# Performance work log

Hardware: AMD Instinct MI355X
Metric: run time of the kernel (lower is better)

The kernel has to match this reference:

```python
import jax, jax.numpy as jnp
import numpy as np

C = 1024
RANK = 8


def _layernorm(x, g, b, eps=1e-5):
    mu = jnp.mean(x, axis=-1, keepdims=True)
    var = jnp.var(x, axis=-1, keepdims=True)
    return (x - mu) * jax.lax.rsqrt(var + eps) * g + b


def setup_inputs() -> dict:
    key = jax.random.key(0)
    ks = jax.random.split(key, 10)
    B, T = 4, 4096
    x = jax.random.normal(ks[0], (B, T, C), dtype=jnp.float32)
    # parameters (match torch inits)
    W0 = jnp.eye(C, dtype=jnp.float32) * 0.1
    A_init = jax.random.normal(ks[1], (C, RANK), dtype=jnp.float32) * 0.01
    B_init = jnp.zeros((RANK, C), dtype=jnp.float32)
    log_lr = jnp.full((C,), float(np.log(0.1)), dtype=jnp.float32)
    s = 1.0 / np.sqrt(C)
    Wq = jax.random.uniform(ks[2], (C, C), minval=-s, maxval=s, dtype=jnp.float32)
    Wk = jax.random.uniform(ks[3], (C, C), minval=-s, maxval=s, dtype=jnp.float32)
    Wv = jax.random.uniform(ks[4], (C, C), minval=-s, maxval=s, dtype=jnp.float32)
    Wo = jax.random.uniform(ks[5], (C, C), minval=-s, maxval=s, dtype=jnp.float32)
    Wg = jax.random.uniform(ks[6], (C, C), minval=-s, maxval=s, dtype=jnp.float32)
    ln_g = jnp.ones((C,), dtype=jnp.float32)
    ln_b = jnp.zeros((C,), dtype=jnp.float32)
    ls_g = jnp.full((C,), 1e-4, dtype=jnp.float32)  # LayerScale gamma
    return {"x": x, "W0": W0, "A_init": A_init, "B_init": B_init,
            "log_lr": log_lr, "Wq": Wq, "Wk": Wk, "Wv": Wv, "Wo": Wo,
            "Wg": Wg, "ln_g": ln_g, "ln_b": ln_b, "ls_g": ls_g}


def reference(x, W0, A_init, B_init, log_lr, Wq, Wk, Wv, Wo, Wg, ln_g, ln_b, ls_g):
    B, T, _ = x.shape
    h = _layernorm(x, ln_g, ln_b)
    # dual-form TTT (training path: q/k/v projections, full K @ W0)
    Q = jnp.einsum('btc,dc->btd', h, Wq)
    K = jnp.einsum('btc,dc->btd', h, Wk)
    V = jnp.einsum('btc,dc->btd', h, Wv)
    lr = jnp.minimum(jnp.exp(log_lr), 1.0)  # clamp(max=1.0)
    y0 = jnp.einsum('btc,cd->btd', K, W0) + jnp.einsum('btr,rd->btd', jnp.einsum('btc,cr->btr', K, A_init), B_init)
    error = y0 - V
    loss = jnp.mean(error ** 2)
    gradient = K * error                     # [B,T,C]
    grad_cumsum = jnp.cumsum(gradient, axis=1)
    grad_shift = jnp.concatenate([jnp.zeros((B, 1, gradient.shape[-1]), gradient.dtype), grad_cumsum[:, :-1, :]], axis=1)
    correction = Q * lr[None, None, :] * grad_shift
    pos = jnp.arange(1, T + 1, dtype=correction.dtype)
    pos_scale = (1.0 / (1.0 + 0.1 * jnp.log(pos)))[None, :, None]
    out = y0 - correction * pos_scale
    # gate, out projection, layer scale, residual
    gate = jax.nn.sigmoid(jnp.einsum('btc,dc->btd', x, Wg))
    out = out * gate
    out = jnp.einsum('btc,dc->btd', out, Wo) * ls_g
    return (x + out, loss)
```

## Files before the change

kernel.cpp:

```cpp
#include <hip/hip_runtime.h>
#include <stdint.h>
#include <math.h>

typedef unsigned short u16;
typedef __attribute__((ext_vector_type(8))) short short8;
typedef __attribute__((ext_vector_type(4))) float f32x4;

__device__ __forceinline__ float bf2f(u16 u){
  union { unsigned int i; float f; } v; v.i = ((unsigned int)u) << 16; return v.f;
}
__device__ __forceinline__ u16 f2bf(float f){
  union { float f; unsigned int i; } v; v.f = f;
  return (u16)((v.i + 0x7FFFu + ((v.i >> 16) & 1u)) >> 16);
}

__global__ void ln_prep(const float* __restrict__ x, const float* __restrict__ g,
                        const float* __restrict__ bta, u16* __restrict__ h,
                        u16* __restrict__ xb, float* __restrict__ loss){
  if (blockIdx.x == 0 && threadIdx.x == 0) loss[0] = 0.f;
  int row = blockIdx.x, tid = threadIdx.x;
  const float4* xr = (const float4*)(x + (size_t)row * 1024);
  float4 v = xr[tid];
  float s  = v.x + v.y + v.z + v.w;
  float s2 = v.x*v.x + v.y*v.y + v.z*v.z + v.w*v.w;
  #pragma unroll
  for (int o = 32; o > 0; o >>= 1){ s += __shfl_down(s, o); s2 += __shfl_down(s2, o); }
  __shared__ float red[8];
  if ((tid & 63) == 0){ red[tid >> 6] = s; red[4 + (tid >> 6)] = s2; }
  __syncthreads();
  float ts = red[0]+red[1]+red[2]+red[3];
  float t2 = red[4]+red[5]+red[6]+red[7];
  float mu   = ts * (1.0f/1024.0f);
  float var  = t2 * (1.0f/1024.0f) - mu*mu;
  float rstd = rsqrtf(var + 1e-5f);
  float4 gg = ((const float4*)g)[tid];
  float4 bb = ((const float4*)bta)[tid];
  ushort4 hv, xv;
  hv.x = f2bf((v.x-mu)*rstd*gg.x + bb.x);
  hv.y = f2bf((v.y-mu)*rstd*gg.y + bb.y);
  hv.z = f2bf((v.z-mu)*rstd*gg.z + bb.z);
  hv.w = f2bf((v.w-mu)*rstd*gg.w + bb.w);
  xv.x = f2bf(v.x); xv.y = f2bf(v.y); xv.z = f2bf(v.z); xv.w = f2bf(v.w);
  ((ushort4*)h )[(size_t)row*256 + tid] = hv;
  ((ushort4*)xb)[(size_t)row*256 + tid] = xv;
}

__global__ void conv5(const float* __restrict__ a, const float* __restrict__ b,
                      const float* __restrict__ c, const float* __restrict__ d,
                      const float* __restrict__ e,
                      u16* oa, u16* ob, u16* oc, u16* od, u16* oe){
  int sel = blockIdx.y;
  const float* s = sel==0?a : sel==1?b : sel==2?c : sel==3?d : e;
  u16* o = sel==0?oa : sel==1?ob : sel==2?oc : sel==3?od : oe;
  int i = blockIdx.x*256 + threadIdx.x;
  float4 v = ((const float4*)s)[i];
  ushort4 r; r.x=f2bf(v.x); r.y=f2bf(v.y); r.z=f2bf(v.z); r.w=f2bf(v.w);
  ((ushort4*)o)[i] = r;
}

__global__ void weff_k(const float* __restrict__ W0, const float* __restrict__ Ai,
                       const float* __restrict__ Bi, u16* __restrict__ Wet){
  __shared__ float tile[32][33];
  int d0 = blockIdx.x*32, e0 = blockIdx.y*32;
  int tid = threadIdx.x;
  int lr = tid >> 5, lc = tid & 31;
  #pragma unroll
  for (int s = 0; s < 4; ++s){
    int e = e0 + s*8 + lr, d = d0 + lc;
    float v = W0[(size_t)e*1024 + d];
    #pragma unroll
    for (int r = 0; r < 8; ++r) v += Ai[e*8 + r] * Bi[(size_t)r*1024 + d];
    tile[s*8 + lr][lc] = v;
  }
  __syncthreads();
  #pragma unroll
  for (int s = 0; s < 4; ++s){
    int d = d0 + s*8 + lr, e = e0 + lc;
    Wet[(size_t)d*1024 + e] = f2bf(tile[lc][s*8 + lr]);
  }
}

template<int EPI>
__device__ __forceinline__ void gemm_body(const u16* __restrict__ A, const u16* __restrict__ Bm,
    u16* __restrict__ Cb, float* __restrict__ Cf, const float* __restrict__ lsg,
    const float* __restrict__ xres, int mblk, int nblk){
  __shared__ u16 As[128*64];
  __shared__ u16 Bs[128*64];
  const int tid  = threadIdx.x;
  const int lane = tid & 63;
  const int w    = tid >> 6;
  const int m0 = mblk * 128, n0 = nblk * 128;
  const int lrow = lane >> 3, lcol8 = (lane & 7) * 8;
  const int wm = w & 1, wn = w >> 1;
  const int l15 = lane & 15, quad = lane >> 4;

  f32x4 acc[4][4] = {};

  #pragma unroll 1
  for (int kk = 0; kk < 1024; kk += 64){
    #pragma unroll
    for (int it = 0; it < 4; ++it){
      int r0 = w*8 + it*32;
      const u16* ga = A  + (size_t)(m0 + r0 + lrow)*1024 + kk + lcol8;
      __builtin_amdgcn_global_load_lds((const __attribute__((address_space(1))) unsigned int*)ga,
          (__attribute__((address_space(3))) unsigned int*)(As + r0*64), 16, 0, 0);
      const u16* gb = Bm + (size_t)(n0 + r0 + lrow)*1024 + kk + lcol8;
      __builtin_amdgcn_global_load_lds((const __attribute__((address_space(1))) unsigned int*)gb,
          (__attribute__((address_space(3))) unsigned int*)(Bs + r0*64), 16, 0, 0);
    }
    __syncthreads();
    #pragma unroll
    for (int kh = 0; kh < 2; ++kh){
      int kb = kh*32 + quad*8;
      short8 af[4], bfv[4];
      #pragma unroll
      for (int i = 0; i < 4; ++i) af[i]  = *(const short8*)(As + (wm*64 + i*16 + l15)*64 + kb);
      #pragma unroll
      for (int j = 0; j < 4; ++j) bfv[j] = *(const short8*)(Bs + (wn*64 + j*16 + l15)*64 + kb);
      #pragma unroll
      for (int i = 0; i < 4; ++i)
        #pragma unroll
        for (int j = 0; j < 4; ++j)
          acc[i][j] = __builtin_amdgcn_mfma_f32_16x16x32_bf16(af[i], bfv[j], acc[i][j], 0, 0, 0);
    }
    __syncthreads();
  }

  const int rbase = quad * 4;
  if (EPI == 0){
    #pragma unroll
    for (int i = 0; i < 4; ++i){
      int row = m0 + wm*64 + i*16 + rbase;
      #pragma unroll
      for (int j = 0; j < 4; ++j){
        int col = n0 + wn*64 + j*16 + l15;
        #pragma unroll
        for (int r = 0; r < 4; ++r)
          Cb[(size_t)(row + r)*1024 + col] = f2bf(acc[i][j][r]);
      }
    }
  } else {
    float lsv[4];
    #pragma unroll
    for (int j = 0; j < 4; ++j) lsv[j] = lsg[n0 + wn*64 + j*16 + l15];
    #pragma unroll
    for (int i = 0; i < 4; ++i){
      int row = m0 + wm*64 + i*16 + rbase;
      #pragma unroll
      for (int j = 0; j < 4; ++j){
        int col = n0 + wn*64 + j*16 + l15;
        #pragma unroll
        for (int r = 0; r < 4; ++r){
          size_t idx = (size_t)(row + r)*1024 + col;
          Cf[idx] = acc[i][j][r] * lsv[j] + xres[idx];
        }
      }
    }
  }
}

__global__ void gemm_qkvg(const u16* __restrict__ h, const u16* __restrict__ xb,
                          const u16* __restrict__ Wqb, const u16* __restrict__ Wkb,
                          const u16* __restrict__ Wvb, const u16* __restrict__ Wgb,
                          u16* __restrict__ Qb, u16* __restrict__ Kb,
                          u16* __restrict__ Vb, u16* __restrict__ Gb){
  int sel = blockIdx.y >> 3;
  const u16* A  = (sel == 3) ? xb : h;
  const u16* Bm = sel==0?Wqb : sel==1?Wkb : sel==2?Wvb : Wgb;
  u16* Out      = sel==0?Qb  : sel==1?Kb  : sel==2?Vb  : Gb;
  gemm_body<0>(A, Bm, Out, nullptr, nullptr, nullptr, blockIdx.x, blockIdx.y & 7);
}

__global__ void gemm_plain(const u16* __restrict__ A, const u16* __restrict__ Bm,
                           u16* __restrict__ C){
  gemm_body<0>(A, Bm, C, nullptr, nullptr, nullptr, blockIdx.x, blockIdx.y);
}

__global__ void gemm_final(const u16* __restrict__ A, const u16* __restrict__ Bm,
                           float* __restrict__ C, const float* __restrict__ lsg,
                           const float* __restrict__ xres){
  gemm_body<1>(A, Bm, nullptr, C, lsg, xres, blockIdx.x, blockIdx.y);
}

__global__ void scan1(const u16* __restrict__ Kb, const u16* __restrict__ Vb,
                      const u16* __restrict__ Yb, float* __restrict__ part,
                      float* __restrict__ loss){
  int tid = threadIdx.x;
  int c = blockIdx.x*256 + tid;
  int ch = blockIdx.y, b = blockIdx.z;
  size_t base = ((size_t)b*4096 + (size_t)ch*128)*1024 + c;
  float g = 0.f, ls = 0.f;
  #pragma unroll 8
  for (int t = 0; t < 128; ++t){
    size_t idx = base + (size_t)t*1024;
    float kv = bf2f(Kb[idx]), vv = bf2f(Vb[idx]), yv = bf2f(Yb[idx]);
    float e = yv - vv;
    g += kv*e; ls += e*e;
  }
  part[((size_t)(b*32 + ch))*1024 + c] = g;
  #pragma unroll
  for (int o = 32; o > 0; o >>= 1) ls += __shfl_down(ls, o);
  __shared__ float red[4];
  if ((tid & 63) == 0) red[tid >> 6] = ls;
  __syncthreads();
  if (tid == 0) atomicAdd(loss, red[0]+red[1]+red[2]+red[3]);
}

__global__ void scan2(const u16* __restrict__ Kb, const u16* __restrict__ Vb,
                      const u16* __restrict__ Yb, const u16* __restrict__ Qb,
                      const u16* __restrict__ Gb, const float* __restrict__ part,
                      const float* __restrict__ llr, u16* __restrict__ OutPre){
  int tid = threadIdx.x;
  int c = blockIdx.x*256 + tid;
  int ch = blockIdx.y, b = blockIdx.z;
  float run = 0.f;
  for (int j = 0; j < ch; ++j) run += part[((size_t)(b*32 + j))*1024 + c];
  float lrc = fminf(expf(llr[c]), 1.0f);
  size_t base = ((size_t)b*4096 + (size_t)ch*128)*1024 + c;
  #pragma unroll 4
  for (int t = 0; t < 128; ++t){
    size_t idx = base + (size_t)t*1024;
    float kv = bf2f(Kb[idx]), vv = bf2f(Vb[idx]), yv = bf2f(Yb[idx]);
    float qv = bf2f(Qb[idx]), gl = bf2f(Gb[idx]);
    float e = yv - vv;
    int tg = ch*128 + t + 1;
    float ps = 1.0f/(1.0f + 0.1f*logf((float)tg));
    float gate = 1.0f/(1.0f + expf(-gl));
    float o = (yv - qv*lrc*run*ps) * gate;
    OutPre[idx] = f2bf(o);
    run += kv*e;
  }
}

__global__ void finloss(const float* __restrict__ loss, float* __restrict__ o){
  o[0] = loss[0] * (1.0f/16777216.0f);
}

extern "C" void kernel_launch(void* const* d_in, const int* in_sizes, int n_in,
                              void* d_out, int out_size, void* d_ws, size_t ws_size,
                              hipStream_t stream){
  const float* x   = (const float*)d_in[0];
  const float* W0  = (const float*)d_in[1];
  const float* Ai  = (const float*)d_in[2];
  const float* Bi  = (const float*)d_in[3];
  const float* llr = (const float*)d_in[4];
  const float* Wq  = (const float*)d_in[5];
  const float* Wk  = (const float*)d_in[6];
  const float* Wv  = (const float*)d_in[7];
  const float* Wo  = (const float*)d_in[8];
  const float* Wg  = (const float*)d_in[9];
  const float* lng = (const float*)d_in[10];
  const float* lnb = (const float*)d_in[11];
  const float* lsg = (const float*)d_in[12];
  float* out = (float*)d_out;

  const size_t TOK = 16384, CC = 1024;
  char* p = (char*)d_ws;
  float* loss = (float*)p; p += 256;
  u16* h   = (u16*)p; p += TOK*CC*2;
  u16* xb  = (u16*)p; p += TOK*CC*2;
  u16* Qb  = (u16*)p; p += TOK*CC*2;
  u16* Kb  = (u16*)p; p += TOK*CC*2;
  u16* Vb  = (u16*)p; p += TOK*CC*2;
  u16* Gb  = (u16*)p; p += TOK*CC*2;
  u16* Wqb = (u16*)p; p += CC*CC*2;
  u16* Wkb = (u16*)p; p += CC*CC*2;
  u16* Wvb = (u16*)p; p += CC*CC*2;
  u16* Wgb = (u16*)p; p += CC*CC*2;
  u16* Wob = (u16*)p; p += CC*CC*2;
  u16* Wet = (u16*)p; p += CC*CC*2;
  float* part = (float*)p; p += (size_t)4*32*1024*4;

  ln_prep<<<16384, 256, 0, stream>>>(x, lng, lnb, h, xb, loss);
  conv5<<<dim3(1024, 5), 256, 0, stream>>>(Wq, Wk, Wv, Wg, Wo, Wqb, Wkb, Wvb, Wgb, Wob);
  weff_k<<<dim3(32, 32), 256, 0, stream>>>(W0, Ai, Bi, Wet);
  gemm_qkvg<<<dim3(128, 32), 256, 0, stream>>>(h, xb, Wqb, Wkb, Wvb, Wgb, Qb, Kb, Vb, Gb);
  gemm_plain<<<dim3(128, 8), 256, 0, stream>>>(Kb, Wet, h);
  scan1<<<dim3(4, 32, 4), 256, 0, stream>>>(Kb, Vb, h, part, loss);
  scan2<<<dim3(4, 32, 4), 256, 0, stream>>>(Kb, Vb, h, Qb, Gb, part, llr, Qb);
  gemm_final<<<dim3(128, 8), 256, 0, stream>>>(Qb, Wob, out, lsg, x);
  finloss<<<1, 1, 0, stream>>>(loss, out + 16777216);
}
```

Baseline: 469.8 us.

## Rewrite GEMMs as 256x256-tile, 4-stage pipelined kernels with swizzled LDS and grid

```diff
diff --git a/kernel.cpp b/kernel.cpp
--- a/kernel.cpp
+++ b/kernel.cpp
@@ -81,56 +81,94 @@
 }
 
 template<int EPI>
-__device__ __forceinline__ void gemm_body(const u16* __restrict__ A, const u16* __restrict__ Bm,
+__device__ __forceinline__ void gemm256_body(const u16* __restrict__ A, const u16* __restrict__ Bm,
     u16* __restrict__ Cb, float* __restrict__ Cf, const float* __restrict__ lsg,
-    const float* __restrict__ xres, int mblk, int nblk){
-  __shared__ u16 As[128*64];
-  __shared__ u16 Bs[128*64];
+    const float* __restrict__ xres, int mblk, int nblk)
+{
+  __shared__ u16 As[4][8192];
+  __shared__ u16 Bs[4][8192];
   const int tid  = threadIdx.x;
   const int lane = tid & 63;
   const int w    = tid >> 6;
-  const int m0 = mblk * 128, n0 = nblk * 128;
-  const int lrow = lane >> 3, lcol8 = (lane & 7) * 8;
-  const int wm = w & 1, wn = w >> 1;
+  const int wm = w >> 2, wn = w & 3;
   const int l15 = lane & 15, quad = lane >> 4;
-
-  f32x4 acc[4][4] = {};
+  const int m0 = mblk * 256, n0 = nblk * 256;
+
+  const int sl   = (lane & 7) ^ (lane >> 3);
+  const int srow = 2*(w*8 + (lane >> 3)) + (sl >> 2);
+  const int scol = (sl & 3) * 8;
+  const u16* gA = A  + (size_t)(m0 + srow)*1024 + scol;
+  const u16* gB = Bm + (size_t)(n0 + srow)*1024 + scol;
+  const int ldsOff = w * 512;
+
+  const int phys8 = (((((l15 & 1) << 2) | quad) ^ (l15 >> 1))) * 8;
+  const int rdA = (wm*64 + (l15 >> 1))*64 + phys8;
+  const int rdB = (wn*32 + (l15 >> 1))*64 + phys8;
+
+  f32x4 acc[8][4] = {};
+
+#define STAGE(T) do{ \
+    const int _s = (T) & 3; \
+    const size_t _k = (size_t)(T) * 32; \
+    __builtin_amdgcn_global_load_lds((const __attribute__((address_space(1))) unsigned int*)(gA + _k), \
+        (__attribute__((address_space(3))) unsigned int*)(&As[_s][ldsOff]), 16, 0, 0); \
+    __builtin_amdgcn_global_load_lds((const __attribute__((address_space(1))) unsigned int*)(gA + _k + 131072), \
+        (__attribute__((address_space(3))) unsigned int*)(&As[_s][ldsOff + 4096]), 16, 0, 0); \
+    __builtin_amdgcn_global_load_lds((const __attribute__((address_space(1))) unsigned int*)(gB + _k), \
+        (__attribute__((address_space(3))) unsigned int*)(&Bs[_s][ldsOff]), 16, 0, 0); \
+    __builtin_amdgcn_global_load_lds((const __attribute__((address_space(1))) unsigned int*)(gB + _k + 131072), \
+        (__attribute__((address_space(3))) unsigned int*)(&Bs[_s][ldsOff + 4096]), 16, 0, 0); \
+  }while(0)
+
+#define COMPUTE(T) do{ \
+    const int _s = (T) & 3; \
+    const u16* _as = &As[_s][0]; \
+    const u16* _bs = &Bs[_s][0]; \
+    short8 afv[8], bfv[4]; \
+    _Pragma("unroll") \
+    for (int _j = 0; _j < 4; ++_j) bfv[_j] = *(const short8*)(_bs + rdB + _j*512); \
+    _Pragma("unroll") \
+    for (int _i = 0; _i < 8; ++_i) afv[_i] = *(const short8*)(_as + rdA + _i*512); \
+    __builtin_amdgcn_s_setprio(1); \
+    _Pragma("unroll") \
+    for (int _i = 0; _i < 8; ++_i){ \
+      _Pragma("unroll") \
+      for (int _j = 0; _j < 4; ++_j) \
+        acc[_i][_j] = __builtin_amdgcn_mfma_f32_16x16x32_bf16(afv[_i], bfv[_j], acc[_i][_j], 0, 0, 0); \
+    } \
+    __builtin_amdgcn_s_setprio(0); \
+  }while(0)
+
+  STAGE(0); STAGE(1); STAGE(2);
 
   #pragma unroll 1
-  for (int kk = 0; kk < 1024; kk += 64){
-    #pragma unroll
-    for (int it = 0; it < 4; ++it){
-      int r0 = w*8 + it*32;
-      const u16* ga = A  + (size_t)(m0 + r0 + lrow)*1024 + kk + lcol8;
-      __builtin_amdgcn_global_load_lds((const __attribute__((address_space(1))) unsigned int*)ga,
-          (__attribute__((address_space(3))) unsigned int*)(As + r0*64), 16, 0, 0);
-      const u16* gb = Bm + (size_t)(n0 + r0 + lrow)*1024 + kk + lcol8;
-      __builtin_amdgcn_global_load_lds((const __attribute__((address_space(1))) unsigned int*)gb,
-          (__attribute__((address_space(3))) unsigned int*)(Bs + r0*64), 16, 0, 0);
-    }
-    __syncthreads();
-    #pragma unroll
-    for (int kh = 0; kh < 2; ++kh){
-      int kb = kh*32 + quad*8;
-      short8 af[4], bfv[4];
-      #pragma unroll
-      for (int i = 0; i < 4; ++i) af[i]  = *(const short8*)(As + (wm*64 + i*16 + l15)*64 + kb);
-      #pragma unroll
-      for (int j = 0; j < 4; ++j) bfv[j] = *(const short8*)(Bs + (wn*64 + j*16 + l15)*64 + kb);
-      #pragma unroll
-      for (int i = 0; i < 4; ++i)
-        #pragma unroll
-        for (int j = 0; j < 4; ++j)
-          acc[i][j] = __builtin_amdgcn_mfma_f32_16x16x32_bf16(af[i], bfv[j], acc[i][j], 0, 0, 0);
-    }
-    __syncthreads();
-  }
+  for (int t = 0; t < 29; ++t){
+    asm volatile("s_waitcnt vmcnt(8)" ::: "memory");
+    __builtin_amdgcn_s_barrier();
+    __builtin_amdgcn_sched_barrier(0);
+    STAGE(t + 3);
+    COMPUTE(t);
+  }
+  asm volatile("s_waitcnt vmcnt(8)" ::: "memory");
+  __builtin_amdgcn_s_barrier();
+  __builtin_amdgcn_sched_barrier(0);
+  COMPUTE(29);
+  asm volatile("s_waitcnt vmcnt(4)" ::: "memory");
+  __builtin_amdgcn_s_barrier();
+  __builtin_amdgcn_sched_barrier(0);
+  COMPUTE(30);
+  asm volatile("s_waitcnt vmcnt(0)" ::: "memory");
+  __builtin_amdgcn_s_barrier();
+  __builtin_amdgcn_sched_barrier(0);
+  COMPUTE(31);
+#undef STAGE
+#undef COMPUTE
 
   const int rbase = quad * 4;
   if (EPI == 0){
     #pragma unroll
-    for (int i = 0; i < 4; ++i){
-      int row = m0 + wm*64 + i*16 + rbase;
+    for (int i = 0; i < 8; ++i){
+      int row = m0 + wm*128 + i*16 + rbase;
       #pragma unroll
       for (int j = 0; j < 4; ++j){
         int col = n0 + wn*64 + j*16 + l15;
@@ -144,8 +182,8 @@
     #pragma unroll
     for (int j = 0; j < 4; ++j) lsv[j] = lsg[n0 + wn*64 + j*16 + l15];
     #pragma unroll
-    for (int i = 0; i < 4; ++i){
-      int row = m0 + wm*64 + i*16 + rbase;
+    for (int i = 0; i < 8; ++i){
+      int row = m0 + wm*128 + i*16 + rbase;
       #pragma unroll
       for (int j = 0; j < 4; ++j){
         int col = n0 + wn*64 + j*16 + l15;
@@ -159,27 +197,37 @@
   }
 }
 
-__global__ void gemm_qkvg(const u16* __restrict__ h, const u16* __restrict__ xb,
-                          const u16* __restrict__ Wqb, const u16* __restrict__ Wkb,
-                          const u16* __restrict__ Wvb, const u16* __restrict__ Wgb,
-                          u16* __restrict__ Qb, u16* __restrict__ Kb,
-                          u16* __restrict__ Vb, u16* __restrict__ Gb){
-  int sel = blockIdx.y >> 3;
+__global__ __launch_bounds__(512, 2) void gemm_qkvg(
+    const u16* __restrict__ h, const u16* __restrict__ xb,
+    const u16* __restrict__ Wqb, const u16* __restrict__ Wkb,
+    const u16* __restrict__ Wvb, const u16* __restrict__ Wgb,
+    u16* __restrict__ Qb, u16* __restrict__ Kb,
+    u16* __restrict__ Vb, u16* __restrict__ Gb){
+  int bid = blockIdx.x;
+  int swz = (bid & 7) * 128 + (bid >> 3);
+  int mblk = swz >> 4;
+  int rem  = swz & 15;
+  int sel  = rem >> 2, nblk = rem & 3;
   const u16* A  = (sel == 3) ? xb : h;
   const u16* Bm = sel==0?Wqb : sel==1?Wkb : sel==2?Wvb : Wgb;
   u16* Out      = sel==0?Qb  : sel==1?Kb  : sel==2?Vb  : Gb;
-  gemm_body<0>(A, Bm, Out, nullptr, nullptr, nullptr, blockIdx.x, blockIdx.y & 7);
-}
-
-__global__ void gemm_plain(const u16* __restrict__ A, const u16* __restrict__ Bm,
-                           u16* __restrict__ C){
-  gemm_body<0>(A, Bm, C, nullptr, nullptr, nullptr, blockIdx.x, blockIdx.y);
-}
-
-__global__ void gemm_final(const u16* __restrict__ A, const u16* __restrict__ Bm,
-                           float* __restrict__ C, const float* __restrict__ lsg,
-                           const float* __restrict__ xres){
-  gemm_body<1>(A, Bm, nullptr, C, lsg, xres, blockIdx.x, blockIdx.y);
+  gemm256_body<0>(A, Bm, Out, nullptr, nullptr, nullptr, mblk, nblk);
+}
+
+__global__ __launch_bounds__(512, 2) void gemm_plain(
+    const u16* __restrict__ A, const u16* __restrict__ Bm, u16* __restrict__ C){
+  int bid = blockIdx.x;
+  int swz = (bid & 7) * 32 + (bid >> 3);
+  gemm256_body<0>(A, Bm, C, nullptr, nullptr, nullptr, swz >> 2, swz & 3);
+}
+
+__global__ __launch_bounds__(512, 2) void gemm_final(
+    const u16* __restrict__ A, const u16* __restrict__ Bm,
+    float* __restrict__ C, const float* __restrict__ lsg,
+    const float* __restrict__ xres){
+  int bid = blockIdx.x;
+  int swz = (bid & 7) * 32 + (bid >> 3);
+  gemm256_body<1>(A, Bm, nullptr, C, lsg, xres, swz >> 2, swz & 3);
 }
 
 __global__ void scan1(const u16* __restrict__ Kb, const u16* __restrict__ Vb,
@@ -274,10 +322,10 @@
   ln_prep<<<16384, 256, 0, stream>>>(x, lng, lnb, h, xb, loss);
   conv5<<<dim3(1024, 5), 256, 0, stream>>>(Wq, Wk, Wv, Wg, Wo, Wqb, Wkb, Wvb, Wgb, Wob);
   weff_k<<<dim3(32, 32), 256, 0, stream>>>(W0, Ai, Bi, Wet);
-  gemm_qkvg<<<dim3(128, 32), 256, 0, stream>>>(h, xb, Wqb, Wkb, Wvb, Wgb, Qb, Kb, Vb, Gb);
-  gemm_plain<<<dim3(128, 8), 256, 0, stream>>>(Kb, Wet, h);
+  gemm_qkvg<<<1024, 512, 0, stream>>>(h, xb, Wqb, Wkb, Wvb, Wgb, Qb, Kb, Vb, Gb);
+  gemm_plain<<<256, 512, 0, stream>>>(Kb, Wet, h);
   scan1<<<dim3(4, 32, 4), 256, 0, stream>>>(Kb, Vb, h, part, loss);
   scan2<<<dim3(4, 32, 4), 256, 0, stream>>>(Kb, Vb, h, Qb, Gb, part, llr, Qb);
-  gemm_final<<<dim3(128, 8), 256, 0, stream>>>(Qb, Wob, out, lsg, x);
+  gemm_final<<<256, 512, 0, stream>>>(Qb, Wob, out, lsg, x);
   finloss<<<1, 1, 0, stream>>>(loss, out + 16777216);
 }
```

Result: slower. 495.7 us (+5.5%).
